# Kernel tuning notes

Measured on AMD Instinct MI355X. Metric: run time of the kernel, lower is better.

## Reference

```python
import jax, jax.numpy as jnp
import numpy as np


def setup_inputs() -> dict:
    key = jax.random.key(0)
    kA, kW = jax.random.split(key, 2)
    T, N = 64, 128  # seq_len, num_peds
    A = jax.random.normal(kA, (T, N, N), dtype=jnp.float32)
    # Linear(2N -> 1): weight stored as (2N, 1), bias (1,)
    W = jax.random.normal(kW, (2 * N, 1), dtype=jnp.float32) * (1.0 / np.sqrt(2 * N))
    b = jnp.zeros((1,), dtype=jnp.float32)
    return {"A": A, "W": W, "b": b}


def reference(A, W, b):
    # A: (T, N, N). Original loops over timesteps; here fully vectorized.
    N = A.shape[2]
    aT = jnp.swapaxes(A, 1, 2)            # a_ = a_.T per timestep -> (T, N, N)
    # Pairwise concat [aT[i], aT[j]] fed to Linear(2N->1) decomposes exactly:
    # score[t,i,j] = aT[t,i]@w1 + aT[t,j]@w2 + b
    w1, w2 = W[:N, 0], W[N:, 0]           # (N,), (N,)
    s1 = aT @ w1                           # (T, N) row-i contribution
    s2 = aT @ w2                           # (T, N) row-j contribution
    e = jax.nn.leaky_relu(s1[:, :, None] + s2[:, None, :] + b[0],
                          negative_slope=0.2)   # (T, N, N)
    alpha = jax.nn.softmax(e, axis=2)      # softmax over neighbor index j (torch dim=1 of (N,N,1))
    # GAT-style aggregation: out[t,i,f] = sum_j alpha[t,i,j] * aT[t,j,f]
    return jnp.einsum('tij,tjf->tif', alpha, aT)
```

## Files before the change

kernel.cpp:

```cpp
#include <hip/hip_runtime.h>

#define NN 128

typedef __attribute__((ext_vector_type(8))) short short8;
typedef __attribute__((ext_vector_type(4))) float f32x4;

__device__ __forceinline__ int SWZ(int r, int cs) {
    return (r << 7) + (cs ^ ((r & 7) << 3));
}

__device__ __forceinline__ unsigned asu(float x) { return __float_as_uint(x); }
__device__ __forceinline__ float asf(unsigned u) { return __uint_as_float(u); }

__global__ __launch_bounds__(256, 2) void gat_fused(
    const float* __restrict__ A, const float* __restrict__ W,
    const float* __restrict__ b, float* __restrict__ out)
{
    __shared__ unsigned short Ah_s[NN * NN];
    __shared__ unsigned short Al_s[NN * NN];
    __shared__ unsigned short ah_s[16 * NN];
    __shared__ unsigned short al_s[16 * NN];
    __shared__ float w_s[2 * NN];
    __shared__ float part1_s[4 * NN];
    __shared__ float part2_s[4 * NN];

    const int tid  = threadIdx.x;
    const int lane = tid & 63;
    const int wid  = tid >> 6;
    const int t    = blockIdx.x & 63;
    const int i0   = (blockIdx.x >> 6) << 4;
    const float* At = A + (size_t)t * NN * NN;
    const float b0 = b[0];

    if (tid < 64)
        reinterpret_cast<float4*>(w_s)[tid] = reinterpret_cast<const float4*>(W)[tid];
    __syncthreads();

    {
        const float4* A4 = reinterpret_cast<const float4*>(At);
        float p1[4] = {0,0,0,0}, p2[4] = {0,0,0,0};
        #pragma unroll
        for (int it = 0; it < 16; ++it) {
            int e4 = it * 256 + tid;
            int f  = e4 >> 5;
            int cs = (e4 & 31) << 2;
            float4 v = A4[e4];
            float wf1 = w_s[f], wf2 = w_s[NN + f];
            p1[0] += wf1 * v.x; p1[1] += wf1 * v.y; p1[2] += wf1 * v.z; p1[3] += wf1 * v.w;
            p2[0] += wf2 * v.x; p2[1] += wf2 * v.y; p2[2] += wf2 * v.z; p2[3] += wf2 * v.w;
            unsigned ux = asu(v.x), uy = asu(v.y), uz = asu(v.z), uw = asu(v.w);
            float rx = v.x - asf(ux & 0xffff0000u);
            float ry = v.y - asf(uy & 0xffff0000u);
            float rz = v.z - asf(uz & 0xffff0000u);
            float rw = v.w - asf(uw & 0xffff0000u);
            uint2 hv, lv;
            hv.x = (ux >> 16) | (uy & 0xffff0000u);
            hv.y = (uz >> 16) | (uw & 0xffff0000u);
            lv.x = (asu(rx) >> 16) | (asu(ry) & 0xffff0000u);
            lv.y = (asu(rz) >> 16) | (asu(rw) & 0xffff0000u);
            int idx = SWZ(f, cs);
            *reinterpret_cast<uint2*>(&Ah_s[idx]) = hv;
            *reinterpret_cast<uint2*>(&Al_s[idx]) = lv;
        }
        #pragma unroll
        for (int q = 0; q < 4; ++q) {
            p1[q] += __shfl_xor(p1[q], 32);
            p2[q] += __shfl_xor(p2[q], 32);
        }
        if (lane < 32) {
            float4 v1 = { p1[0], p1[1], p1[2], p1[3] };
            float4 v2 = { p2[0], p2[1], p2[2], p2[3] };
            *reinterpret_cast<float4*>(&part1_s[wid * NN + lane * 4]) = v1;
            *reinterpret_cast<float4*>(&part2_s[wid * NN + lane * 4]) = v2;
        }
    }
    __syncthreads();

    {
        int r  = tid >> 4;
        int jj = tid & 15;
        float s1v = part1_s[i0 + r] + part1_s[NN + i0 + r]
                  + part1_s[2 * NN + i0 + r] + part1_s[3 * NN + i0 + r] + b0;
        float s2v[8] = {0,0,0,0,0,0,0,0};
        #pragma unroll
        for (int w = 0; w < 4; ++w) {
            float4 a = *reinterpret_cast<const float4*>(&part2_s[w * NN + jj * 8]);
            float4 c = *reinterpret_cast<const float4*>(&part2_s[w * NN + jj * 8 + 4]);
            s2v[0] += a.x; s2v[1] += a.y; s2v[2] += a.z; s2v[3] += a.w;
            s2v[4] += c.x; s2v[5] += c.y; s2v[6] += c.z; s2v[7] += c.w;
        }
        float ev[8];
        float m = -3.4e38f;
        #pragma unroll
        for (int c = 0; c < 8; ++c) {
            float x = s1v + s2v[c];
            x = (x >= 0.f) ? x : 0.2f * x;
            ev[c] = x;
            m = fmaxf(m, x);
        }
        m = fmaxf(m, __shfl_xor(m, 1));
        m = fmaxf(m, __shfl_xor(m, 2));
        m = fmaxf(m, __shfl_xor(m, 4));
        m = fmaxf(m, __shfl_xor(m, 8));
        float s = 0.f;
        #pragma unroll
        for (int c = 0; c < 8; ++c) { ev[c] = __expf(ev[c] - m); s += ev[c]; }
        s += __shfl_xor(s, 1);
        s += __shfl_xor(s, 2);
        s += __shfl_xor(s, 4);
        s += __shfl_xor(s, 8);
        float inv = 1.0f / s;
        unsigned h[4], l[4];
        #pragma unroll
        for (int c = 0; c < 8; c += 2) {
            float v0 = ev[c] * inv, v1 = ev[c + 1] * inv;
            unsigned u0 = asu(v0), u1 = asu(v1);
            float r0 = v0 - asf(u0 & 0xffff0000u);
            float r1 = v1 - asf(u1 & 0xffff0000u);
            h[c >> 1] = (u0 >> 16) | (u1 & 0xffff0000u);
            l[c >> 1] = (asu(r0) >> 16) | (asu(r1) & 0xffff0000u);
        }
        int idx = SWZ(r, jj * 8);
        uint4 hv = { h[0], h[1], h[2], h[3] };
        uint4 lv = { l[0], l[1], l[2], l[3] };
        *reinterpret_cast<uint4*>(&ah_s[idx]) = hv;
        *reinterpret_cast<uint4*>(&al_s[idx]) = lv;
    }
    __syncthreads();

    {
        int f0 = wid * 32;
        int ar = lane & 15;
        int kg = (lane >> 4) << 3;
        f32x4 acc0 = {0.f,0.f,0.f,0.f}, acc1 = {0.f,0.f,0.f,0.f};
        const unsigned short* aps[3] = { ah_s, ah_s, al_s };
        const unsigned short* bps[3] = { Ah_s, Al_s, Ah_s };
        #pragma unroll
        for (int pass = 0; pass < 3; ++pass) {
            const unsigned short* ap = aps[pass];
            const unsigned short* bp = bps[pass];
            #pragma unroll
            for (int k0 = 0; k0 < NN; k0 += 32) {
                short8 a  = *reinterpret_cast<const short8*>(&ap[SWZ(ar, k0 + kg)]);
                short8 bb0 = *reinterpret_cast<const short8*>(&bp[SWZ(f0 + ar, k0 + kg)]);
                short8 bb1 = *reinterpret_cast<const short8*>(&bp[SWZ(f0 + 16 + ar, k0 + kg)]);
                acc0 = __builtin_amdgcn_mfma_f32_16x16x32_bf16(a, bb0, acc0, 0, 0, 0);
                acc1 = __builtin_amdgcn_mfma_f32_16x16x32_bf16(a, bb1, acc1, 0, 0, 0);
            }
        }
        float* outt = out + (size_t)t * NN * NN;
        int orow = i0 + ((lane >> 4) << 2);
        int col  = lane & 15;
        #pragma unroll
        for (int q = 0; q < 4; ++q) {
            outt[(orow + q) * NN + f0 + col]      = acc0[q];
            outt[(orow + q) * NN + f0 + 16 + col] = acc1[q];
        }
    }
}

extern "C" void kernel_launch(void* const* d_in, const int* in_sizes, int n_in,
                              void* d_out, int out_size, void* d_ws, size_t ws_size,
                              hipStream_t stream) {
    const float* A = (const float*)d_in[0];
    const float* W = (const float*)d_in[1];
    const float* b = (const float*)d_in[2];
    float* out = (float*)d_out;
    gat_fused<<<dim3(512), dim3(256), 0, stream>>>(A, W, b, out);
}
```

Measured before the change: 10.96 us.

## Compute softmax attention directly in MFMA A-fragment registers, skip LDS staging

Each wave now computes the softmax row values itself, in the exact MFMA A-operand layout. It packs them into bf16 hi/lo fragments in registers instead of writing alpha to shared memory and reading it back. A small s1/s2 reduction step into LDS replaces the per-thread partial sums. The B fragments are preloaded into registers once and reused across the three split-bf16 passes, which removes the redundant B reloads. The cost is redundant softmax and exp work across the four waves (each does all 16 rows × 128 columns) and higher register pressure.

```diff
diff --git a/kernel.cpp b/kernel.cpp
--- a/kernel.cpp
+++ b/kernel.cpp
@@ -18,11 +18,9 @@
 {
     __shared__ unsigned short Ah_s[NN * NN];
     __shared__ unsigned short Al_s[NN * NN];
-    __shared__ unsigned short ah_s[16 * NN];
-    __shared__ unsigned short al_s[16 * NN];
     __shared__ float w_s[2 * NN];
-    __shared__ float part1_s[4 * NN];
-    __shared__ float part2_s[4 * NN];
+    __shared__ float part1_s[4 * NN], part2_s[4 * NN];
+    __shared__ float s1_s[NN], s2_s[NN];
 
     const int tid  = threadIdx.x;
     const int lane = tid & 63;
@@ -76,78 +74,93 @@
     }
     __syncthreads();
 
-    {
-        int r  = tid >> 4;
-        int jj = tid & 15;
-        float s1v = part1_s[i0 + r] + part1_s[NN + i0 + r]
-                  + part1_s[2 * NN + i0 + r] + part1_s[3 * NN + i0 + r] + b0;
-        float s2v[8] = {0,0,0,0,0,0,0,0};
-        #pragma unroll
-        for (int w = 0; w < 4; ++w) {
-            float4 a = *reinterpret_cast<const float4*>(&part2_s[w * NN + jj * 8]);
-            float4 c = *reinterpret_cast<const float4*>(&part2_s[w * NN + jj * 8 + 4]);
-            s2v[0] += a.x; s2v[1] += a.y; s2v[2] += a.z; s2v[3] += a.w;
-            s2v[4] += c.x; s2v[5] += c.y; s2v[6] += c.z; s2v[7] += c.w;
-        }
-        float ev[8];
-        float m = -3.4e38f;
-        #pragma unroll
-        for (int c = 0; c < 8; ++c) {
-            float x = s1v + s2v[c];
-            x = (x >= 0.f) ? x : 0.2f * x;
-            ev[c] = x;
-            m = fmaxf(m, x);
-        }
-        m = fmaxf(m, __shfl_xor(m, 1));
-        m = fmaxf(m, __shfl_xor(m, 2));
-        m = fmaxf(m, __shfl_xor(m, 4));
-        m = fmaxf(m, __shfl_xor(m, 8));
-        float s = 0.f;
-        #pragma unroll
-        for (int c = 0; c < 8; ++c) { ev[c] = __expf(ev[c] - m); s += ev[c]; }
-        s += __shfl_xor(s, 1);
-        s += __shfl_xor(s, 2);
-        s += __shfl_xor(s, 4);
-        s += __shfl_xor(s, 8);
-        float inv = 1.0f / s;
-        unsigned h[4], l[4];
-        #pragma unroll
-        for (int c = 0; c < 8; c += 2) {
-            float v0 = ev[c] * inv, v1 = ev[c + 1] * inv;
-            unsigned u0 = asu(v0), u1 = asu(v1);
-            float r0 = v0 - asf(u0 & 0xffff0000u);
-            float r1 = v1 - asf(u1 & 0xffff0000u);
-            h[c >> 1] = (u0 >> 16) | (u1 & 0xffff0000u);
-            l[c >> 1] = (asu(r0) >> 16) | (asu(r1) & 0xffff0000u);
-        }
-        int idx = SWZ(r, jj * 8);
-        uint4 hv = { h[0], h[1], h[2], h[3] };
-        uint4 lv = { l[0], l[1], l[2], l[3] };
-        *reinterpret_cast<uint4*>(&ah_s[idx]) = hv;
-        *reinterpret_cast<uint4*>(&al_s[idx]) = lv;
+    if (tid < NN) {
+        s1_s[tid] = part1_s[tid] + part1_s[NN + tid]
+                  + part1_s[2 * NN + tid] + part1_s[3 * NN + tid] + b0;
+        s2_s[tid] = part2_s[tid] + part2_s[NN + tid]
+                  + part2_s[2 * NN + tid] + part2_s[3 * NN + tid];
     }
     __syncthreads();
 
     {
-        int f0 = wid * 32;
-        int ar = lane & 15;
-        int kg = (lane >> 4) << 3;
-        f32x4 acc0 = {0.f,0.f,0.f,0.f}, acc1 = {0.f,0.f,0.f,0.f};
-        const unsigned short* aps[3] = { ah_s, ah_s, al_s };
-        const unsigned short* bps[3] = { Ah_s, Al_s, Ah_s };
+        const int f0 = wid * 32;
+        const int ar = lane & 15;
+        const int kg = (lane >> 4) << 3;
+
+        short8 bh0[4], bh1[4], bl0[4], bl1[4];
         #pragma unroll
-        for (int pass = 0; pass < 3; ++pass) {
-            const unsigned short* ap = aps[pass];
-            const unsigned short* bp = bps[pass];
+        for (int k = 0; k < 4; ++k) {
+            int c = k * 32 + kg;
+            bh0[k] = *reinterpret_cast<const short8*>(&Ah_s[SWZ(f0 + ar, c)]);
+            bh1[k] = *reinterpret_cast<const short8*>(&Ah_s[SWZ(f0 + 16 + ar, c)]);
+            bl0[k] = *reinterpret_cast<const short8*>(&Al_s[SWZ(f0 + ar, c)]);
+            bl1[k] = *reinterpret_cast<const short8*>(&Al_s[SWZ(f0 + 16 + ar, c)]);
+        }
+
+        float s1v = s1_s[i0 + ar];
+        float ev[32];
+        float m = -3.4e38f;
+        #pragma unroll
+        for (int k = 0; k < 4; ++k) {
+            float4 sa = *reinterpret_cast<const float4*>(&s2_s[k * 32 + kg]);
+            float4 sb = *reinterpret_cast<const float4*>(&s2_s[k * 32 + kg + 4]);
+            float xs[8] = { sa.x, sa.y, sa.z, sa.w, sb.x, sb.y, sb.z, sb.w };
             #pragma unroll
-            for (int k0 = 0; k0 < NN; k0 += 32) {
-                short8 a  = *reinterpret_cast<const short8*>(&ap[SWZ(ar, k0 + kg)]);
-                short8 bb0 = *reinterpret_cast<const short8*>(&bp[SWZ(f0 + ar, k0 + kg)]);
-                short8 bb1 = *reinterpret_cast<const short8*>(&bp[SWZ(f0 + 16 + ar, k0 + kg)]);
-                acc0 = __builtin_amdgcn_mfma_f32_16x16x32_bf16(a, bb0, acc0, 0, 0, 0);
-                acc1 = __builtin_amdgcn_mfma_f32_16x16x32_bf16(a, bb1, acc1, 0, 0, 0);
+            for (int e = 0; e < 8; ++e) {
+                float x = s1v + xs[e];
+                x = (x >= 0.f) ? x : 0.2f * x;
+                ev[k * 8 + e] = x;
+                m = fmaxf(m, x);
             }
         }
+        m = fmaxf(m, __shfl_xor(m, 16));
+        m = fmaxf(m, __shfl_xor(m, 32));
+        float s = 0.f;
+        #pragma unroll
+        for (int c = 0; c < 32; ++c) { ev[c] = __expf(ev[c] - m); s += ev[c]; }
+        s += __shfl_xor(s, 16);
+        s += __shfl_xor(s, 32);
+        float inv = 1.0f / s;
+
+        short8 ah[4], al[4];
+        #pragma unroll
+        for (int k = 0; k < 4; ++k) {
+            union { short8 s8; uint4 u4; } H, L;
+            #pragma unroll
+            for (int p = 0; p < 4; ++p) {
+                float v0 = ev[k * 8 + 2 * p]     * inv;
+                float v1 = ev[k * 8 + 2 * p + 1] * inv;
+                unsigned u0 = asu(v0), u1 = asu(v1);
+                float r0 = v0 - asf(u0 & 0xffff0000u);
+                float r1 = v1 - asf(u1 & 0xffff0000u);
+                unsigned hw = (u0 >> 16) | (u1 & 0xffff0000u);
+                unsigned lw = (asu(r0) >> 16) | (asu(r1) & 0xffff0000u);
+                if (p == 0) { H.u4.x = hw; L.u4.x = lw; }
+                else if (p == 1) { H.u4.y = hw; L.u4.y = lw; }
+                else if (p == 2) { H.u4.z = hw; L.u4.z = lw; }
+                else { H.u4.w = hw; L.u4.w = lw; }
+            }
+            ah[k] = H.s8;
+            al[k] = L.s8;
+        }
+
+        f32x4 acc0 = {0.f,0.f,0.f,0.f}, acc1 = {0.f,0.f,0.f,0.f};
+        #pragma unroll
+        for (int k = 0; k < 4; ++k) {
+            acc0 = __builtin_amdgcn_mfma_f32_16x16x32_bf16(ah[k], bh0[k], acc0, 0, 0, 0);
+            acc1 = __builtin_amdgcn_mfma_f32_16x16x32_bf16(ah[k], bh1[k], acc1, 0, 0, 0);
+        }
+        #pragma unroll
+        for (int k = 0; k < 4; ++k) {
+            acc0 = __builtin_amdgcn_mfma_f32_16x16x32_bf16(ah[k], bl0[k], acc0, 0, 0, 0);
+            acc1 = __builtin_amdgcn_mfma_f32_16x16x32_bf16(ah[k], bl1[k], acc1, 0, 0, 0);
+        }
+        #pragma unroll
+        for (int k = 0; k < 4; ++k) {
+            acc0 = __builtin_amdgcn_mfma_f32_16x16x32_bf16(al[k], bh0[k], acc0, 0, 0, 0);
+            acc1 = __builtin_amdgcn_mfma_f32_16x16x32_bf16(al[k], bh1[k], acc1, 0, 0, 0);
+        }
+
         float* outt = out + (size_t)t * NN * NN;
         int orow = i0 + ((lane >> 4) << 2);
         int col  = lane & 15;
```

After: 11.64 us. 1.06x slower.

## Drop low-bf16 A tile from LDS, build it in registers from a global reload

Applied to the files above, without the earlier changes.

Removes the Al_s shared-memory tile (32 KB) and the W staging buffer, so occupancy can rise to 3 blocks per CU. The low-residual bf16 fragments of A used as the B operand are now computed in registers from a second global (likely cache-hit) load of A rows. The s1/s2 reductions are done once into shared arrays instead of per thread. In exchange it adds an extra sync, extra global traffic and more register pressure under the tighter launch bound.

```diff
diff --git a/kernel.cpp b/kernel.cpp
--- a/kernel.cpp
+++ b/kernel.cpp
@@ -12,17 +12,23 @@
 __device__ __forceinline__ unsigned asu(float x) { return __float_as_uint(x); }
 __device__ __forceinline__ float asf(unsigned u) { return __uint_as_float(u); }
 
-__global__ __launch_bounds__(256, 2) void gat_fused(
+__device__ __forceinline__ unsigned pk_hi(float v0, float v1) {
+    return (asu(v0) >> 16) | (asu(v1) & 0xffff0000u);
+}
+__device__ __forceinline__ float resid(float x) {
+    return x - asf(asu(x) & 0xffff0000u);
+}
+
+__global__ __launch_bounds__(256, 3) void gat_fused(
     const float* __restrict__ A, const float* __restrict__ W,
     const float* __restrict__ b, float* __restrict__ out)
 {
     __shared__ unsigned short Ah_s[NN * NN];
-    __shared__ unsigned short Al_s[NN * NN];
     __shared__ unsigned short ah_s[16 * NN];
     __shared__ unsigned short al_s[16 * NN];
-    __shared__ float w_s[2 * NN];
     __shared__ float part1_s[4 * NN];
     __shared__ float part2_s[4 * NN];
+    __shared__ float s1_s[NN], s2_s[NN];
 
     const int tid  = threadIdx.x;
     const int lane = tid & 63;
@@ -30,11 +36,6 @@
     const int t    = blockIdx.x & 63;
     const int i0   = (blockIdx.x >> 6) << 4;
     const float* At = A + (size_t)t * NN * NN;
-    const float b0 = b[0];
-
-    if (tid < 64)
-        reinterpret_cast<float4*>(w_s)[tid] = reinterpret_cast<const float4*>(W)[tid];
-    __syncthreads();
 
     {
         const float4* A4 = reinterpret_cast<const float4*>(At);
@@ -45,22 +46,13 @@
             int f  = e4 >> 5;
             int cs = (e4 & 31) << 2;
             float4 v = A4[e4];
-            float wf1 = w_s[f], wf2 = w_s[NN + f];
-            p1[0] += wf1 * v.x; p1[1] += wf1 * v.y; p1[2] += wf1 * v.z; p1[3] += wf1 * v.w;
-            p2[0] += wf2 * v.x; p2[1] += wf2 * v.y; p2[2] += wf2 * v.z; p2[3] += wf2 * v.w;
-            unsigned ux = asu(v.x), uy = asu(v.y), uz = asu(v.z), uw = asu(v.w);
-            float rx = v.x - asf(ux & 0xffff0000u);
-            float ry = v.y - asf(uy & 0xffff0000u);
-            float rz = v.z - asf(uz & 0xffff0000u);
-            float rw = v.w - asf(uw & 0xffff0000u);
-            uint2 hv, lv;
-            hv.x = (ux >> 16) | (uy & 0xffff0000u);
-            hv.y = (uz >> 16) | (uw & 0xffff0000u);
-            lv.x = (asu(rx) >> 16) | (asu(ry) & 0xffff0000u);
-            lv.y = (asu(rz) >> 16) | (asu(rw) & 0xffff0000u);
-            int idx = SWZ(f, cs);
-            *reinterpret_cast<uint2*>(&Ah_s[idx]) = hv;
-            *reinterpret_cast<uint2*>(&Al_s[idx]) = lv;
+            float w1 = W[f], w2 = W[NN + f];
+            p1[0] += w1 * v.x; p1[1] += w1 * v.y; p1[2] += w1 * v.z; p1[3] += w1 * v.w;
+            p2[0] += w2 * v.x; p2[1] += w2 * v.y; p2[2] += w2 * v.z; p2[3] += w2 * v.w;
+            uint2 hv;
+            hv.x = pk_hi(v.x, v.y);
+            hv.y = pk_hi(v.z, v.w);
+            *reinterpret_cast<uint2*>(&Ah_s[SWZ(f, cs)]) = hv;
         }
         #pragma unroll
         for (int q = 0; q < 4; ++q) {
@@ -76,24 +68,44 @@
     }
     __syncthreads();
 
+    const int f0 = wid << 5;
+    const int r  = lane & 15;
+    const int g  = lane >> 4;
+    const int kg = g << 3;
+
+    const float* Brow0 = At + (size_t)(f0 + r) * NN + kg;
+    const float* Brow1 = At + (size_t)(f0 + 16 + r) * NN + kg;
+    float4 bv0[8], bv1[8];
+    #pragma unroll
+    for (int k = 0; k < 4; ++k) {
+        bv0[2 * k]     = *reinterpret_cast<const float4*>(Brow0 + 32 * k);
+        bv0[2 * k + 1] = *reinterpret_cast<const float4*>(Brow0 + 32 * k + 4);
+        bv1[2 * k]     = *reinterpret_cast<const float4*>(Brow1 + 32 * k);
+        bv1[2 * k + 1] = *reinterpret_cast<const float4*>(Brow1 + 32 * k + 4);
+    }
+
+    if (tid < NN) {
+        s1_s[tid] = part1_s[tid] + part1_s[NN + tid]
+                  + part1_s[2 * NN + tid] + part1_s[3 * NN + tid] + b[0];
+    } else {
+        int c = tid - NN;
+        s2_s[c] = part2_s[c] + part2_s[NN + c]
+                + part2_s[2 * NN + c] + part2_s[3 * NN + c];
+    }
+    __syncthreads();
+
     {
-        int r  = tid >> 4;
+        int rr = tid >> 4;
         int jj = tid & 15;
-        float s1v = part1_s[i0 + r] + part1_s[NN + i0 + r]
-                  + part1_s[2 * NN + i0 + r] + part1_s[3 * NN + i0 + r] + b0;
-        float s2v[8] = {0,0,0,0,0,0,0,0};
-        #pragma unroll
-        for (int w = 0; w < 4; ++w) {
-            float4 a = *reinterpret_cast<const float4*>(&part2_s[w * NN + jj * 8]);
-            float4 c = *reinterpret_cast<const float4*>(&part2_s[w * NN + jj * 8 + 4]);
-            s2v[0] += a.x; s2v[1] += a.y; s2v[2] += a.z; s2v[3] += a.w;
-            s2v[4] += c.x; s2v[5] += c.y; s2v[6] += c.z; s2v[7] += c.w;
-        }
+        float s1v = s1_s[i0 + rr];
+        float4 sa = *reinterpret_cast<const float4*>(&s2_s[jj * 8]);
+        float4 sb = *reinterpret_cast<const float4*>(&s2_s[jj * 8 + 4]);
+        float xs[8] = { sa.x, sa.y, sa.z, sa.w, sb.x, sb.y, sb.z, sb.w };
         float ev[8];
         float m = -3.4e38f;
         #pragma unroll
         for (int c = 0; c < 8; ++c) {
-            float x = s1v + s2v[c];
+            float x = s1v + xs[c];
             x = (x >= 0.f) ? x : 0.2f * x;
             ev[c] = x;
             m = fmaxf(m, x);
@@ -114,48 +126,58 @@
         #pragma unroll
         for (int c = 0; c < 8; c += 2) {
             float v0 = ev[c] * inv, v1 = ev[c + 1] * inv;
-            unsigned u0 = asu(v0), u1 = asu(v1);
-            float r0 = v0 - asf(u0 & 0xffff0000u);
-            float r1 = v1 - asf(u1 & 0xffff0000u);
-            h[c >> 1] = (u0 >> 16) | (u1 & 0xffff0000u);
-            l[c >> 1] = (asu(r0) >> 16) | (asu(r1) & 0xffff0000u);
+            h[c >> 1] = pk_hi(v0, v1);
+            l[c >> 1] = pk_hi(resid(v0), resid(v1));
         }
-        int idx = SWZ(r, jj * 8);
+        int idx = SWZ(rr, jj * 8);
         uint4 hv = { h[0], h[1], h[2], h[3] };
         uint4 lv = { l[0], l[1], l[2], l[3] };
         *reinterpret_cast<uint4*>(&ah_s[idx]) = hv;
         *reinterpret_cast<uint4*>(&al_s[idx]) = lv;
     }
+
+    short8 bl0[4], bl1[4];
+    #pragma unroll
+    for (int k = 0; k < 4; ++k) {
+        union { short8 s8; unsigned u[4]; } L0, L1;
+        L0.u[0] = pk_hi(resid(bv0[2 * k].x),     resid(bv0[2 * k].y));
+        L0.u[1] = pk_hi(resid(bv0[2 * k].z),     resid(bv0[2 * k].w));
+        L0.u[2] = pk_hi(resid(bv0[2 * k + 1].x), resid(bv0[2 * k + 1].y));
+        L0.u[3] = pk_hi(resid(bv0[2 * k + 1].z), resid(bv0[2 * k + 1].w));
+        L1.u[0] = pk_hi(resid(bv1[2 * k].x),     resid(bv1[2 * k].y));
+        L1.u[1] = pk_hi(resid(bv1[2 * k].z),     resid(bv1[2 * k].w));
+        L1.u[2] = pk_hi(resid(bv1[2 * k + 1].x), resid(bv1[2 * k + 1].y));
+        L1.u[3] = pk_hi(resid(bv1[2 * k + 1].z), resid(bv1[2 * k + 1].w));
+        bl0[k] = L0.s8; bl1[k] = L1.s8;
+    }
     __syncthreads();
 
-    {
-        int f0 = wid * 32;
-        int ar = lane & 15;
-        int kg = (lane >> 4) << 3;
-        f32x4 acc0 = {0.f,0.f,0.f,0.f}, acc1 = {0.f,0.f,0.f,0.f};
-        const unsigned short* aps[3] = { ah_s, ah_s, al_s };
-        const unsigned short* bps[3] = { Ah_s, Al_s, Ah_s };
-        #pragma unroll
-        for (int pass = 0; pass < 3; ++pass) {
-            const unsigned short* ap = aps[pass];
-            const unsigned short* bp = bps[pass];
-            #pragma unroll
-            for (int k0 = 0; k0 < NN; k0 += 32) {
-                short8 a  = *reinterpret_cast<const short8*>(&ap[SWZ(ar, k0 + kg)]);
-                short8 bb0 = *reinterpret_cast<const short8*>(&bp[SWZ(f0 + ar, k0 + kg)]);
-                short8 bb1 = *reinterpret_cast<const short8*>(&bp[SWZ(f0 + 16 + ar, k0 + kg)]);
-                acc0 = __builtin_amdgcn_mfma_f32_16x16x32_bf16(a, bb0, acc0, 0, 0, 0);
-                acc1 = __builtin_amdgcn_mfma_f32_16x16x32_bf16(a, bb1, acc1, 0, 0, 0);
-            }
-        }
-        float* outt = out + (size_t)t * NN * NN;
-        int orow = i0 + ((lane >> 4) << 2);
-        int col  = lane & 15;
-        #pragma unroll
-        for (int q = 0; q < 4; ++q) {
-            outt[(orow + q) * NN + f0 + col]      = acc0[q];
-            outt[(orow + q) * NN + f0 + 16 + col] = acc1[q];
-        }
+    f32x4 acc0 = {0.f,0.f,0.f,0.f}, acc1 = {0.f,0.f,0.f,0.f};
+    #pragma unroll
+    for (int k0 = 0; k0 < 4; ++k0) {
+        int c = k0 * 32 + kg;
+        short8 ahk = *reinterpret_cast<const short8*>(&ah_s[SWZ(r, c)]);
+        short8 alk = *reinterpret_cast<const short8*>(&al_s[SWZ(r, c)]);
+        short8 bh0 = *reinterpret_cast<const short8*>(&Ah_s[SWZ(f0 + r, c)]);
+        short8 bh1 = *reinterpret_cast<const short8*>(&Ah_s[SWZ(f0 + 16 + r, c)]);
+        acc0 = __builtin_amdgcn_mfma_f32_16x16x32_bf16(ahk, bh0, acc0, 0, 0, 0);
+        acc1 = __builtin_amdgcn_mfma_f32_16x16x32_bf16(ahk, bh1, acc1, 0, 0, 0);
+        acc0 = __builtin_amdgcn_mfma_f32_16x16x32_bf16(alk, bh0, acc0, 0, 0, 0);
+        acc1 = __builtin_amdgcn_mfma_f32_16x16x32_bf16(alk, bh1, acc1, 0, 0, 0);
+    }
+    #pragma unroll
+    for (int k0 = 0; k0 < 4; ++k0) {
+        int c = k0 * 32 + kg;
+        short8 ahk = *reinterpret_cast<const short8*>(&ah_s[SWZ(r, c)]);
+        acc0 = __builtin_amdgcn_mfma_f32_16x16x32_bf16(ahk, bl0[k0], acc0, 0, 0, 0);
+        acc1 = __builtin_amdgcn_mfma_f32_16x16x32_bf16(ahk, bl1[k0], acc1, 0, 0, 0);
+    }
+
+    float* outt = out + (size_t)t * NN * NN + (size_t)(i0 + (g << 2)) * NN;
+    #pragma unroll
+    for (int q = 0; q < 4; ++q) {
+        outt[q * NN + f0 + r]      = acc0[q];
+        outt[q * NN + f0 + 16 + r] = acc1[q];
     }
 }
 
```

Result: slower. 12.94 us (+18.1%).
